# Performance work log

Hardware: AMD Instinct MI355X
Metric: run time of the kernel (lower is better)

## Reference

```python
import jax, jax.numpy as jnp
import numpy as np

N = 50000        # total nodes across batch
K = 16           # max neighbors per node (padded with index 0)
E = 800000       # directed edges / messages
B = 1024         # molecules
MAXM = 48        # max nodes per molecule (padded with index 0)
FEATURE_FDIM = 9
ALL_FDIM = 10    # feature_dist_graph (9) + reshaped rij distance (1)
H = 64           # hidden_dim
NUM_ITERS = 2
NEG_INF = -1e9


def setup_inputs() -> dict:
    key = jax.random.key(0)
    ks = jax.random.split(key, 16)
    s = 1.0 / np.sqrt(H)
    return {
        "target_features": jax.random.normal(ks[0], (N, FEATURE_FDIM), jnp.float32),
        "feature_dist_graph": jax.random.normal(ks[1], (E, ALL_FDIM - 1), jnp.float32),
        "rij_dist_pairs": jax.random.uniform(ks[2], (E,), jnp.float32),
        "start_end_env": jax.random.randint(ks[3], (N, K), 0, N + 1),
        "b_scope": jax.random.randint(ks[4], (N, K), 0, E),
        "l_scope": jax.random.randint(ks[5], (B, MAXM), 0, N + 1),
        "scope_update": jax.random.randint(ks[6], (E,), 0, N + 1),
        "scope_update_lig": jax.random.randint(ks[7], (E,), 0, N + 1),
        "W_emb": jax.random.uniform(ks[8], (FEATURE_FDIM, H), jnp.float32, 0.1, 0.9),
        "b_emb": jnp.zeros((H,), jnp.float32),
        "W_dist": jax.random.uniform(ks[9], (ALL_FDIM, H), jnp.float32, 0.1, 0.9),
        "b_dist": jnp.zeros((H,), jnp.float32),
        "W_gat": jax.random.normal(ks[10], (H, H), jnp.float32) * s,
        "Wm_gat": jax.random.normal(ks[11], (H, H), jnp.float32) * s,
        "a_gat": jax.random.normal(ks[12], (2 * H,), jnp.float32) * s,
    }


def reference(target_features, feature_dist_graph, rij_dist_pairs,
              start_end_env, b_scope, l_scope, scope_update, scope_update_lig,
              W_emb, b_emb, W_dist, b_dist, W_gat, Wm_gat, a_gat):
    # node embedding over origin features
    h = target_features @ W_emb + b_emb                        # [N, H]
    # edge message embedding over pair features + distance
    msg_in = jnp.concatenate([feature_dist_graph, rij_dist_pairs[:, None]], axis=1)
    message = msg_in @ W_dist + b_dist                         # [E, H]
    # prepend zero pad row (index 0 = padding for ragged gathers)
    hp = jnp.concatenate([jnp.zeros((1, H), h.dtype), h], axis=0)  # [N+1, H]
    pad_mask = (start_end_env == 0)                            # [N, K]
    upd_mask = (scope_update_lig > 0).astype(h.dtype)[:, None]  # [E, 1]
    for _ in range(NUM_ITERS):
        nb = hp[start_end_env]                                 # [N, K, H] gather neighbors
        mg = message[b_scope]                                  # [N, K, H] gather messages
        Wn = nb @ W_gat                                        # [N, K, H]
        Wm = mg @ Wm_gat                                       # [N, K, H]
        # GAT attention logits: leaky_relu(a^T [Wn || Wm])
        logits = jax.nn.leaky_relu(
            jnp.einsum('nkh,h->nk', Wn, a_gat[:H]) +
            jnp.einsum('nkh,h->nk', Wm, a_gat[H:]), 0.2)       # [N, K]
        logits = jnp.where(pad_mask, NEG_INF, logits)
        alpha = jax.nn.softmax(logits, axis=1)                 # [N, K]
        new_h = jax.nn.elu(jnp.einsum('nk,nkh->nh', alpha, Wn + Wm))  # [N, H]
        hp = jnp.concatenate([jnp.zeros((1, H), new_h.dtype), new_h], axis=0)
        # scatter updated node features back into edge messages
        message = hp[scope_update] * upd_mask                  # [E, H]
    cmp_enc = hp[l_scope]                                      # [B, MAXM, H]
    return cmp_enc.sum(axis=1)                                 # [B, H]
```

## Files before the change

kernel.cpp:

```cpp
#include <hip/hip_runtime.h>
#include <hip/hip_bf16.h>

#define N_NODES 50000
#define K_NB 16
#define E_EDGES 800000
#define B_MOL 1024
#define MAXM_M 48
#define FDIM 9
#define ADIM 10
#define H 64
#define NEG_INF_F (-1e9f)
#define PRE_NODE_BLOCKS 196
#define EDGE_BLOCKS 3125

__device__ inline float readlane_f(float v, int l) {
    return __int_as_float(__builtin_amdgcn_readlane(__float_as_int(v), l));
}
__device__ inline int readlane_i(int v, int l) {
    return __builtin_amdgcn_readlane(v, l);
}
__device__ inline unsigned readlane_u(unsigned v, int l) {
    return (unsigned)__builtin_amdgcn_readlane((int)v, l);
}
__device__ inline float bf2f(unsigned u) {
    return __uint_as_float(u << 16);
}
__device__ inline float bf2f_lo(unsigned u) { return __uint_as_float(u << 16); }
__device__ inline float bf2f_hi(unsigned u) { return __uint_as_float(u & 0xffff0000u); }
__device__ inline unsigned short f2bf(float f) {
    unsigned x = __float_as_uint(f);
    return (unsigned short)((x + 0x7fffu + ((x >> 16) & 1u)) >> 16);
}

#define GLOAD_U16(dst, voff, sbase) \
    asm volatile("global_load_ushort %0, %1, %2" : "=v"(dst) : "v"(voff), "s"(sbase))
#define GLOAD_F32(dst, voff, sbase) \
    asm volatile("global_load_dword %0, %1, %2" : "=v"(dst) : "v"(voff), "s"(sbase))

#define DRAIN16(a) \
    asm volatile("s_waitcnt vmcnt(0)" \
        : "+v"(a[0]), "+v"(a[1]), "+v"(a[2]), "+v"(a[3]), \
          "+v"(a[4]), "+v"(a[5]), "+v"(a[6]), "+v"(a[7]), \
          "+v"(a[8]), "+v"(a[9]), "+v"(a[10]), "+v"(a[11]), \
          "+v"(a[12]), "+v"(a[13]), "+v"(a[14]), "+v"(a[15]))
#define HOLD16(a) \
    asm volatile("" \
        : "+v"(a[0]), "+v"(a[1]), "+v"(a[2]), "+v"(a[3]), \
          "+v"(a[4]), "+v"(a[5]), "+v"(a[6]), "+v"(a[7]), \
          "+v"(a[8]), "+v"(a[9]), "+v"(a[10]), "+v"(a[11]), \
          "+v"(a[12]), "+v"(a[13]), "+v"(a[14]), "+v"(a[15]))

__global__ __launch_bounds__(256) void k_fold(
    const float* __restrict__ W_emb, const float* __restrict__ b_emb,
    const float* __restrict__ W_dist, const float* __restrict__ b_dist,
    const float* __restrict__ W_gat, const float* __restrict__ Wm_gat,
    const float* __restrict__ a_gat,
    float* __restrict__ W2, float* __restrict__ c2,
    float* __restrict__ W3, float* __restrict__ c3,
    float* __restrict__ wa, float* __restrict__ ca,
    float* __restrict__ va, float* __restrict__ vb,
    float* __restrict__ wv9, float* __restrict__ cv)
{
    __shared__ float s_va[64], s_vb[64];
    int tid = threadIdx.x;
    int h = tid & 63, g = tid >> 6;
    if (g == 0) {
        float acc = 0.f;
        for (int t = 0; t < H; ++t) acc += W_gat[h * H + t] * a_gat[t];
        s_va[h] = acc; va[h] = acc;
    } else if (g == 1) {
        float acc = 0.f;
        for (int t = 0; t < H; ++t) acc += Wm_gat[h * H + t] * a_gat[H + t];
        s_vb[h] = acc; vb[h] = acc;
    } else if (g == 2) {
        float acc = 0.f;
        for (int t = 0; t < H; ++t) acc += b_dist[t] * Wm_gat[t * H + h];
        c2[h] = acc;
    } else {
        float acc = 0.f;
        for (int t = 0; t < H; ++t) acc += b_emb[t] * W_gat[t * H + h];
        c3[h] = acc;
    }
    __syncthreads();
    for (int q = tid; q < 640; q += 256) {
        int j = q >> 6, hh = q & 63;
        float acc = 0.f;
        for (int t = 0; t < H; ++t) acc += W_dist[j * H + t] * Wm_gat[t * H + hh];
        W2[q] = acc;
    }
    for (int q = tid; q < 576; q += 256) {
        int j = q >> 6, hh = q & 63;
        float acc = 0.f;
        for (int t = 0; t < H; ++t) acc += W_emb[j * H + t] * W_gat[t * H + hh];
        W3[q] = acc;
    }
    if (tid < ADIM) {
        float acc = 0.f;
        for (int t = 0; t < H; ++t) acc += W_dist[tid * H + t] * s_vb[t];
        wa[tid] = acc;
    } else if (tid == ADIM) {
        float acc = 0.f;
        for (int t = 0; t < H; ++t) acc += b_dist[t] * s_vb[t];
        ca[0] = acc;
    } else if (tid >= 16 && tid < 16 + FDIM) {
        int j = tid - 16;
        float acc = 0.f;
        for (int t = 0; t < H; ++t) acc += W_emb[j * H + t] * s_va[t];
        wv9[j] = acc;
    } else if (tid == 31) {
        float acc = 0.f;
        for (int t = 0; t < H; ++t) acc += b_emb[t] * s_va[t];
        cv[0] = acc;
    }
}

__global__ __launch_bounds__(256) void k_pre(
    const float* __restrict__ tf, const float* __restrict__ fdg,
    const float* __restrict__ rij,
    const int* __restrict__ su, const int* __restrict__ sul,
    const float* __restrict__ wa, const float* __restrict__ ca,
    const float* __restrict__ wv9, const float* __restrict__ cv,
    float* __restrict__ t1A, unsigned short* __restrict__ tfp,
    unsigned short* __restrict__ emsg, int* __restrict__ sue)
{
    int bid = blockIdx.x;
    if (bid < PRE_NODE_BLOCKS) {
        int n = bid * 256 + threadIdx.x;
        if (n == 0) {
            t1A[0] = 0.f;
            uint4 z = make_uint4(0, 0, 0, 0);
            ((uint4*)tfp)[0] = z; ((uint4*)tfp)[1] = z;
        }
        if (n >= N_NODES) return;
        float f[FDIM];
        float acc = cv[0];
#pragma unroll
        for (int j = 0; j < FDIM; ++j) {
            f[j] = tf[n * FDIM + j];
            acc += f[j] * wv9[j];
        }
        t1A[n + 1] = acc;
        unsigned rec[8];
#pragma unroll
        for (int j = 0; j < 4; ++j)
            rec[j] = (unsigned)f2bf(f[2 * j]) | ((unsigned)f2bf(f[2 * j + 1]) << 16);
        rec[4] = (unsigned)f2bf(f[8]);
        rec[5] = 0; rec[6] = 0; rec[7] = 0;
        uint4* dst = (uint4*)(tfp + (size_t)(n + 1) * 16);
        dst[0] = make_uint4(rec[0], rec[1], rec[2], rec[3]);
        dst[1] = make_uint4(rec[4], rec[5], rec[6], rec[7]);
    } else {
        int e = (bid - PRE_NODE_BLOCKS) * 256 + threadIdx.x;
        float f[ADIM];
#pragma unroll
        for (int j = 0; j < FDIM; ++j) f[j] = fdg[(size_t)e * FDIM + j];
        f[FDIM] = rij[e];
        float acc = ca[0];
#pragma unroll
        for (int j = 0; j < ADIM; ++j) acc += f[j] * wa[j];
        unsigned rec[8];
#pragma unroll
        for (int j = 0; j < 5; ++j)
            rec[j] = (unsigned)f2bf(f[2 * j]) | ((unsigned)f2bf(f[2 * j + 1]) << 16);
        rec[5] = __float_as_uint(acc);
        rec[6] = 0; rec[7] = 0;
        uint4* dst = (uint4*)(emsg + (size_t)e * 16);
        dst[0] = make_uint4(rec[0], rec[1], rec[2], rec[3]);
        dst[1] = make_uint4(rec[4], rec[5], rec[6], rec[7]);
        sue[e] = (sul[e] > 0) ? su[e] : 0;
    }
}

__global__ __launch_bounds__(256) void k_gat1(
    const int* __restrict__ sse, const int* __restrict__ bsc,
    const float* __restrict__ t1A, const unsigned short* __restrict__ tfp,
    const unsigned short* __restrict__ emsg,
    const float* __restrict__ W2, const float* __restrict__ c2,
    const float* __restrict__ W3, const float* __restrict__ c3,
    const float* __restrict__ va, const float* __restrict__ vb,
    unsigned short* __restrict__ hp2bf, float* __restrict__ t1B,
    float* __restrict__ t2B)
{
    int wave = threadIdx.x >> 6;
    int lane = threadIdx.x & 63;
    int n = blockIdx.x * 4 + wave;
    if (n == 0) {
        hp2bf[lane] = 0;
        if (lane == 0) { t1B[0] = 0.f; t2B[0] = 0.f; }
    }
    if (n >= N_NODES) return;

    int kidx = 0, ke = 0;
    float lg = NEG_INF_F;
    if (lane < K_NB) {
        kidx = sse[n * K_NB + lane];
        ke   = bsc[n * K_NB + lane];
        float g2 = __uint_as_float(*(const unsigned*)(emsg + (size_t)ke * 16 + 10));
        float p = t1A[kidx] + g2;
        p = (p > 0.f) ? p : 0.2f * p;
        lg = (kidx == 0) ? NEG_INF_F : p;
    }

    unsigned wn_u[K_NB], wm_u[K_NB];
    int offr = (lane & 15) * 2;
#pragma unroll
    for (int k = 0; k < K_NB; ++k) {
        const unsigned short* pk = tfp + (size_t)readlane_i(kidx, k) * 16;
        GLOAD_U16(wn_u[k], offr, pk);
    }
#pragma unroll
    for (int k = 0; k < K_NB; ++k) {
        const unsigned short* pe = emsg + (size_t)readlane_i(ke, k) * 16;
        GLOAD_U16(wm_u[k], offr, pe);
    }

    float m = lg;
#pragma unroll
    for (int o = 8; o > 0; o >>= 1) m = fmaxf(m, __shfl_xor(m, o, 64));
    float ex = __expf(lg - m);
    float s = ex;
#pragma unroll
    for (int o = 8; o > 0; o >>= 1) s += __shfl_xor(s, o, 64);
    float alpha = ex / s;

    DRAIN16(wn_u);
    HOLD16(wm_u);

    float fr = 0.f, frm = 0.f, beta = 0.f;
#pragma unroll
    for (int k = 0; k < K_NB; ++k) {
        float ak = readlane_f(alpha, k);
        fr  += ak * bf2f(wn_u[k]);
        frm += ak * bf2f(wm_u[k]);
        beta += (readlane_i(kidx, k) > 0) ? ak : 0.f;
    }
    float acc = c2[lane] + beta * c3[lane];
#pragma unroll
    for (int j = 0; j < FDIM; ++j) acc += readlane_f(fr, j) * W3[j * H + lane];
#pragma unroll
    for (int j = 0; j < ADIM; ++j) acc += readlane_f(frm, j) * W2[j * H + lane];
    float o = (acc > 0.f) ? acc : expm1f(acc);
    hp2bf[(size_t)(n + 1) * H + lane] = f2bf(o);
    float ta = o * va[lane], tb = o * vb[lane];
#pragma unroll
    for (int q = 32; q > 0; q >>= 1) {
        ta += __shfl_xor(ta, q, 64);
        tb += __shfl_xor(tb, q, 64);
    }
    if (lane == 0) { t1B[n + 1] = ta; t2B[n + 1] = tb; }
}

__global__ __launch_bounds__(256) void k_gat2(
    const int* __restrict__ sse, const int* __restrict__ bsc,
    const int* __restrict__ sue,
    const float* __restrict__ t1B, const float* __restrict__ t2B,
    const unsigned short* __restrict__ hp2bf,
    unsigned* __restrict__ gnm)
{
    int wave = threadIdx.x >> 6;
    int lane = threadIdx.x & 63;
    int n = blockIdx.x * 4 + wave;
    if (n == 0) gnm[lane] = 0;
    if (n >= N_NODES) return;

    int kidx = 0, ksu = 0;
    float lg = NEG_INF_F;
    if (lane < K_NB) {
        kidx = sse[n * K_NB + lane];
        int ke = bsc[n * K_NB + lane];
        ksu = sue[ke];
        float p = t1B[kidx] + t2B[ksu];
        p = (p > 0.f) ? p : 0.2f * p;
        lg = (kidx == 0) ? NEG_INF_F : p;
    }

    unsigned wn_u[K_NB], wm_u[K_NB];
    int off = lane * 2;
#pragma unroll
    for (int k = 0; k < K_NB; ++k) {
        const unsigned short* pk = hp2bf + (size_t)readlane_i(kidx, k) * H;
        GLOAD_U16(wn_u[k], off, pk);
    }
#pragma unroll
    for (int k = 0; k < K_NB; ++k) {
        const unsigned short* ps = hp2bf + (size_t)readlane_i(ksu, k) * H;
        GLOAD_U16(wm_u[k], off, ps);
    }

    float m = lg;
#pragma unroll
    for (int o = 8; o > 0; o >>= 1) m = fmaxf(m, __shfl_xor(m, o, 64));
    float ex = __expf(lg - m);
    float s = ex;
#pragma unroll
    for (int o = 8; o > 0; o >>= 1) s += __shfl_xor(s, o, 64);
    float alpha = ex / s;

    DRAIN16(wn_u);
    HOLD16(wm_u);

    float gn = 0.f, gm = 0.f;
#pragma unroll
    for (int k = 0; k < K_NB; ++k) {
        float ak = readlane_f(alpha, k);
        gn += ak * bf2f(wn_u[k]);
        gm += ak * bf2f(wm_u[k]);
    }
    gnm[(size_t)(n + 1) * H + lane] =
        (unsigned)f2bf(gn) | ((unsigned)f2bf(gm) << 16);
}

__global__ __launch_bounds__(256) void k_proj(
    const unsigned* __restrict__ gnm,
    const float* __restrict__ W_gat, const float* __restrict__ Wm_gat,
    float* __restrict__ hp3)
{
    int lane = threadIdx.x & 63;
    float wg[H], wm[H];
#pragma unroll
    for (int j = 0; j < H; ++j) {
        wg[j] = W_gat[j * H + lane];
        wm[j] = Wm_gat[j * H + lane];
    }
    int wid = blockIdx.x * 4 + (threadIdx.x >> 6);
    int stride2 = gridDim.x * 4 * 2;
    for (int row = wid * 2; row <= N_NODES; row += stride2) {
        int row1 = row + 1;
        bool has1 = (row1 <= N_NODES);
        unsigned u0 = gnm[(size_t)row * H + lane];
        unsigned u1 = has1 ? gnm[(size_t)row1 * H + lane] : 0u;
        float an0 = 0.f, am0 = 0.f, an1 = 0.f, am1 = 0.f;
#pragma unroll
        for (int j = 0; j < H; ++j) {
            unsigned a = readlane_u(u0, j);
            unsigned b = readlane_u(u1, j);
            an0 += bf2f_lo(a) * wg[j];
            am0 += bf2f_hi(a) * wm[j];
            an1 += bf2f_lo(b) * wg[j];
            am1 += bf2f_hi(b) * wm[j];
        }
        float acc0 = an0 + am0;
        hp3[(size_t)row * H + lane] = (acc0 > 0.f) ? acc0 : expm1f(acc0);
        if (has1) {
            float acc1 = an1 + am1;
            hp3[(size_t)row1 * H + lane] = (acc1 > 0.f) ? acc1 : expm1f(acc1);
        }
    }
}

__global__ __launch_bounds__(256) void k_out(
    const int* __restrict__ l_scope, const float* __restrict__ hp,
    float* __restrict__ out)
{
    int wave = threadIdx.x >> 6;
    int lane = threadIdx.x & 63;
    int b = blockIdx.x * 4 + wave;
    if (b >= B_MOL) return;
    int idx48 = (lane < MAXM_M) ? l_scope[b * MAXM_M + lane] : 0;
    float v[MAXM_M];
    int off = lane * 4;
#pragma unroll
    for (int m = 0; m < MAXM_M; ++m) {
        const float* pm = hp + (size_t)readlane_i(idx48, m) * H;
        GLOAD_F32(v[m], off, pm);
    }
    asm volatile("s_waitcnt vmcnt(0)"
        : "+v"(v[0]), "+v"(v[1]), "+v"(v[2]), "+v"(v[3]),
          "+v"(v[4]), "+v"(v[5]), "+v"(v[6]), "+v"(v[7]),
          "+v"(v[8]), "+v"(v[9]), "+v"(v[10]), "+v"(v[11]),
          "+v"(v[12]), "+v"(v[13]), "+v"(v[14]), "+v"(v[15]));
    asm volatile(""
        : "+v"(v[16]), "+v"(v[17]), "+v"(v[18]), "+v"(v[19]),
          "+v"(v[20]), "+v"(v[21]), "+v"(v[22]), "+v"(v[23]),
          "+v"(v[24]), "+v"(v[25]), "+v"(v[26]), "+v"(v[27]),
          "+v"(v[28]), "+v"(v[29]), "+v"(v[30]), "+v"(v[31]));
    asm volatile(""
        : "+v"(v[32]), "+v"(v[33]), "+v"(v[34]), "+v"(v[35]),
          "+v"(v[36]), "+v"(v[37]), "+v"(v[38]), "+v"(v[39]),
          "+v"(v[40]), "+v"(v[41]), "+v"(v[42]), "+v"(v[43]),
          "+v"(v[44]), "+v"(v[45]), "+v"(v[46]), "+v"(v[47]));
    float acc = 0.f;
#pragma unroll
    for (int m = 0; m < MAXM_M; ++m) acc += v[m];
    out[b * H + lane] = acc;
}

extern "C" void kernel_launch(void* const* d_in, const int* in_sizes, int n_in,
                              void* d_out, int out_size, void* d_ws, size_t ws_size,
                              hipStream_t stream)
{
    const float* tf     = (const float*)d_in[0];
    const float* fdg    = (const float*)d_in[1];
    const float* rij    = (const float*)d_in[2];
    const int*   sse    = (const int*)d_in[3];
    const int*   bsc    = (const int*)d_in[4];
    const int*   lsc    = (const int*)d_in[5];
    const int*   su     = (const int*)d_in[6];
    const int*   sul    = (const int*)d_in[7];
    const float* W_emb  = (const float*)d_in[8];
    const float* b_emb  = (const float*)d_in[9];
    const float* W_dist = (const float*)d_in[10];
    const float* b_dist = (const float*)d_in[11];
    const float* W_gat  = (const float*)d_in[12];
    const float* Wm_gat = (const float*)d_in[13];
    const float* a_gat  = (const float*)d_in[14];
    float* out = (float*)d_out;

    char* base = (char*)d_ws;
    size_t off = 0;
    auto alloc = [&](size_t bytes) {
        char* p = base + off;
        off = (off + bytes + 255) & ~(size_t)255;
        return p;
    };
    float* W2   = (float*)alloc(640 * 4);
    float* c2   = (float*)alloc(64 * 4);
    float* W3   = (float*)alloc(640 * 4);
    float* c3   = (float*)alloc(64 * 4);
    float* wa   = (float*)alloc(16 * 4);
    float* ca   = (float*)alloc(16 * 4);
    float* va   = (float*)alloc(64 * 4);
    float* vb   = (float*)alloc(64 * 4);
    float* wv9  = (float*)alloc(16 * 4);
    float* cv   = (float*)alloc(16 * 4);
    float* t1A  = (float*)alloc((size_t)(N_NODES + 1) * 4);
    float* t1B  = (float*)alloc((size_t)(N_NODES + 1) * 4);
    float* t2B  = (float*)alloc((size_t)(N_NODES + 1) * 4);
    int*   sue  = (int*)alloc((size_t)E_EDGES * 4);
    unsigned short* tfp   = (unsigned short*)alloc((size_t)(N_NODES + 1) * 16 * 2);
    unsigned short* hp2bf = (unsigned short*)alloc((size_t)(N_NODES + 1) * H * 2);
    unsigned* gnm = (unsigned*)alloc((size_t)(N_NODES + 1) * H * 4);
    char* big = alloc((size_t)E_EDGES * 32);
    unsigned short* emsg = (unsigned short*)big;
    float* hp3 = (float*)big;

    k_fold<<<dim3(1), dim3(256), 0, stream>>>(
        W_emb, b_emb, W_dist, b_dist, W_gat, Wm_gat, a_gat,
        W2, c2, W3, c3, wa, ca, va, vb, wv9, cv);

    k_pre<<<dim3(PRE_NODE_BLOCKS + EDGE_BLOCKS), dim3(256), 0, stream>>>(
        tf, fdg, rij, su, sul, wa, ca, wv9, cv, t1A, tfp, emsg, sue);

    dim3 gat_grid((N_NODES + 3) / 4);
    k_gat1<<<gat_grid, dim3(256), 0, stream>>>(
        sse, bsc, t1A, tfp, emsg, W2, c2, W3, c3, va, vb, hp2bf, t1B, t2B);

    k_gat2<<<gat_grid, dim3(256), 0, stream>>>(
        sse, bsc, sue, t1B, t2B, hp2bf, gnm);

    k_proj<<<dim3(1024), dim3(256), 0, stream>>>(gnm, W_gat, Wm_gat, hp3);

    k_out<<<dim3(B_MOL / 4), dim3(256), 0, stream>>>(lsc, hp3, out);
}
```

Before: 223.5 us.

## Pack four nodes per wave in first GAT kernel; stage projection weights in LDS

k_gat1 now handles four nodes per wavefront, each in a 16-lane group. All 64 lanes load neighbor and edge indices and gather the 16-element bf16 rows with per-lane pointers, where the old code left 48 lanes idle. Attention weights and the beta sum are reduced within each group, and the per-lane W2/W3 weights are loaded once into registers and reused for all four nodes. k_proj reads W_gat and Wm_gat from shared memory instead of keeping 128 weights per lane in registers, trading LDS reads for lower register pressure and higher occupancy. The gat1 grid becomes N/16, which relies on N being a multiple of 16.

Result: slower. 249.5 us (+11.6%).

```diff
diff --git a/kernel.cpp b/kernel.cpp
--- a/kernel.cpp
+++ b/kernel.cpp
@@ -36,6 +36,8 @@
     asm volatile("global_load_ushort %0, %1, %2" : "=v"(dst) : "v"(voff), "s"(sbase))
 #define GLOAD_F32(dst, voff, sbase) \
     asm volatile("global_load_dword %0, %1, %2" : "=v"(dst) : "v"(voff), "s"(sbase))
+#define GLOADP_U16(dst, ptr) \
+    asm volatile("global_load_ushort %0, %1, off" : "=v"(dst) : "v"(ptr))
 
 #define DRAIN16(a) \
     asm volatile("s_waitcnt vmcnt(0)" \
@@ -183,35 +185,30 @@
 {
     int wave = threadIdx.x >> 6;
     int lane = threadIdx.x & 63;
-    int n = blockIdx.x * 4 + wave;
-    if (n == 0) {
+    int pos  = lane & 15;
+    int gbase = lane & 48;
+    int n0   = blockIdx.x * 16 + wave * 4;
+    if (blockIdx.x == 0 && wave == 0) {
         hp2bf[lane] = 0;
         if (lane == 0) { t1B[0] = 0.f; t2B[0] = 0.f; }
     }
-    if (n >= N_NODES) return;
-
-    int kidx = 0, ke = 0;
-    float lg = NEG_INF_F;
-    if (lane < K_NB) {
-        kidx = sse[n * K_NB + lane];
-        ke   = bsc[n * K_NB + lane];
-        float g2 = __uint_as_float(*(const unsigned*)(emsg + (size_t)ke * 16 + 10));
-        float p = t1A[kidx] + g2;
-        p = (p > 0.f) ? p : 0.2f * p;
-        lg = (kidx == 0) ? NEG_INF_F : p;
-    }
+
+    int kidx = sse[n0 * K_NB + lane];
+    int ke   = bsc[n0 * K_NB + lane];
+    float g2 = __uint_as_float(*(const unsigned*)(emsg + (size_t)(unsigned)ke * 16 + 10));
+    float p  = t1A[kidx] + g2;
+    p = (p > 0.f) ? p : 0.2f * p;
+    float lg = (kidx == 0) ? NEG_INF_F : p;
 
     unsigned wn_u[K_NB], wm_u[K_NB];
-    int offr = (lane & 15) * 2;
 #pragma unroll
     for (int k = 0; k < K_NB; ++k) {
-        const unsigned short* pk = tfp + (size_t)readlane_i(kidx, k) * 16;
-        GLOAD_U16(wn_u[k], offr, pk);
-    }
-#pragma unroll
-    for (int k = 0; k < K_NB; ++k) {
-        const unsigned short* pe = emsg + (size_t)readlane_i(ke, k) * 16;
-        GLOAD_U16(wm_u[k], offr, pe);
+        int idxk = __shfl(kidx, gbase | k, 64);
+        int ek   = __shfl(ke,   gbase | k, 64);
+        const unsigned short* pk = tfp  + ((size_t)(unsigned)idxk * 16u + (unsigned)pos);
+        const unsigned short* pe = emsg + ((size_t)(unsigned)ek   * 16u + (unsigned)pos);
+        GLOADP_U16(wn_u[k], pk);
+        GLOADP_U16(wm_u[k], pe);
     }
 
     float m = lg;
@@ -222,32 +219,48 @@
 #pragma unroll
     for (int o = 8; o > 0; o >>= 1) s += __shfl_xor(s, o, 64);
     float alpha = ex / s;
+    float beta = (kidx == 0) ? 0.f : alpha;
+#pragma unroll
+    for (int o = 8; o > 0; o >>= 1) beta += __shfl_xor(beta, o, 64);
 
     DRAIN16(wn_u);
     HOLD16(wm_u);
 
-    float fr = 0.f, frm = 0.f, beta = 0.f;
+    float frn = 0.f, frm = 0.f;
 #pragma unroll
     for (int k = 0; k < K_NB; ++k) {
-        float ak = readlane_f(alpha, k);
-        fr  += ak * bf2f(wn_u[k]);
+        float ak = __shfl(alpha, gbase | k, 64);
+        frn += ak * bf2f(wn_u[k]);
         frm += ak * bf2f(wm_u[k]);
-        beta += (readlane_i(kidx, k) > 0) ? ak : 0.f;
-    }
-    float acc = c2[lane] + beta * c3[lane];
-#pragma unroll
-    for (int j = 0; j < FDIM; ++j) acc += readlane_f(fr, j) * W3[j * H + lane];
-#pragma unroll
-    for (int j = 0; j < ADIM; ++j) acc += readlane_f(frm, j) * W2[j * H + lane];
-    float o = (acc > 0.f) ? acc : expm1f(acc);
-    hp2bf[(size_t)(n + 1) * H + lane] = f2bf(o);
-    float ta = o * va[lane], tb = o * vb[lane];
-#pragma unroll
-    for (int q = 32; q > 0; q >>= 1) {
-        ta += __shfl_xor(ta, q, 64);
-        tb += __shfl_xor(tb, q, 64);
-    }
-    if (lane == 0) { t1B[n + 1] = ta; t2B[n + 1] = tb; }
+    }
+
+    float w3r[FDIM], w2r[ADIM];
+#pragma unroll
+    for (int j = 0; j < FDIM; ++j) w3r[j] = W3[j * H + lane];
+#pragma unroll
+    for (int j = 0; j < ADIM; ++j) w2r[j] = W2[j * H + lane];
+    float c2r = c2[lane], c3r = c3[lane];
+    float var = va[lane], vbr = vb[lane];
+
+#pragma unroll
+    for (int g = 0; g < 4; ++g) {
+        float acc = c2r + readlane_f(beta, g * 16) * c3r;
+#pragma unroll
+        for (int j = 0; j < FDIM; ++j)
+            acc += readlane_f(frn, g * 16 + j) * w3r[j];
+#pragma unroll
+        for (int j = 0; j < ADIM; ++j)
+            acc += readlane_f(frm, g * 16 + j) * w2r[j];
+        float o = (acc > 0.f) ? acc : expm1f(acc);
+        hp2bf[(size_t)(n0 + g + 1) * H + lane] = f2bf(o);
+        float ta = o * var, tb = o * vbr;
+#pragma unroll
+        for (int q = 32; q > 0; q >>= 1) {
+            ta += __shfl_xor(ta, q, 64);
+            tb += __shfl_xor(tb, q, 64);
+        }
+        if (lane == 0) { t1B[n0 + g + 1] = ta; t2B[n0 + g + 1] = tb; }
+    }
 }
 
 __global__ __launch_bounds__(256) void k_gat2(
@@ -315,13 +328,14 @@
     const float* __restrict__ W_gat, const float* __restrict__ Wm_gat,
     float* __restrict__ hp3)
 {
+    __shared__ float s_wg[H * H];
+    __shared__ float s_wm[H * H];
+    for (int q = threadIdx.x; q < H * H; q += 256) {
+        s_wg[q] = W_gat[q];
+        s_wm[q] = Wm_gat[q];
+    }
+    __syncthreads();
     int lane = threadIdx.x & 63;
-    float wg[H], wm[H];
-#pragma unroll
-    for (int j = 0; j < H; ++j) {
-        wg[j] = W_gat[j * H + lane];
-        wm[j] = Wm_gat[j * H + lane];
-    }
     int wid = blockIdx.x * 4 + (threadIdx.x >> 6);
     int stride2 = gridDim.x * 4 * 2;
     for (int row = wid * 2; row <= N_NODES; row += stride2) {
@@ -332,12 +346,14 @@
         float an0 = 0.f, am0 = 0.f, an1 = 0.f, am1 = 0.f;
 #pragma unroll
         for (int j = 0; j < H; ++j) {
+            float wgj = s_wg[j * H + lane];
+            float wmj = s_wm[j * H + lane];
             unsigned a = readlane_u(u0, j);
             unsigned b = readlane_u(u1, j);
-            an0 += bf2f_lo(a) * wg[j];
-            am0 += bf2f_hi(a) * wm[j];
-            an1 += bf2f_lo(b) * wg[j];
-            am1 += bf2f_hi(b) * wm[j];
+            an0 += bf2f_lo(a) * wgj;
+            am0 += bf2f_hi(a) * wmj;
+            an1 += bf2f_lo(b) * wgj;
+            am1 += bf2f_hi(b) * wmj;
         }
         float acc0 = an0 + am0;
         hp3[(size_t)row * H + lane] = (acc0 > 0.f) ? acc0 : expm1f(acc0);
@@ -441,11 +457,10 @@
     k_pre<<<dim3(PRE_NODE_BLOCKS + EDGE_BLOCKS), dim3(256), 0, stream>>>(
         tf, fdg, rij, su, sul, wa, ca, wv9, cv, t1A, tfp, emsg, sue);
 
-    dim3 gat_grid((N_NODES + 3) / 4);
-    k_gat1<<<gat_grid, dim3(256), 0, stream>>>(
+    k_gat1<<<dim3(N_NODES / 16), dim3(256), 0, stream>>>(
         sse, bsc, t1A, tfp, emsg, W2, c2, W3, c3, va, vb, hp2bf, t1B, t2B);
 
-    k_gat2<<<gat_grid, dim3(256), 0, stream>>>(
+    k_gat2<<<dim3((N_NODES + 3) / 4), dim3(256), 0, stream>>>(
         sse, bsc, sue, t1B, t2B, hp2bf, gnm);
 
     k_proj<<<dim3(1024), dim3(256), 0, stream>>>(gnm, W_gat, Wm_gat, hp3);
```
